# Optimization experiments

Hardware: AMD Instinct MI355X
Metric: run time of the kernel (lower is better)

Reference implementation:

```python
import jax, jax.numpy as jnp
import numpy as np

D_MODEL = 1024
HEADS = 16


def setup_inputs() -> dict:
    key = jax.random.key(0)
    ks = jax.random.split(key, 11)
    B, S, D = 2, 2048, D_MODEL
    scale = 1.0 / np.sqrt(D)
    inp = {
        "q": jax.random.normal(ks[0], (B, S, D), jnp.float32),
        "k": jax.random.normal(ks[1], (B, S, D), jnp.float32),
        "v": jax.random.normal(ks[2], (B, S, D), jnp.float32),
        "w_q": jax.random.normal(ks[3], (D, D), jnp.float32) * scale,
        "b_q": jnp.zeros((D,), jnp.float32),
        "w_k": jax.random.normal(ks[4], (D, D), jnp.float32) * scale,
        "b_k": jnp.zeros((D,), jnp.float32),
        "w_v": jax.random.normal(ks[5], (D, D), jnp.float32) * scale,
        "b_v": jnp.zeros((D,), jnp.float32),
        "w_o": jax.random.normal(ks[6], (D, D), jnp.float32) * scale,
        "b_o": jnp.zeros((D,), jnp.float32),
    }
    return inp


def reference(q, k, v, w_q, b_q, w_k, b_k, w_v, b_v, w_o, b_o):
    B, S, D = q.shape
    H = HEADS
    Dh = D // H

    def split(x):  # [B,S,D] -> [B,H,S,Dh]
        return x.reshape(B, S, H, Dh).transpose(0, 2, 1, 3)

    qh = split(q @ w_q + b_q)
    kh = split(k @ w_k + b_k)
    vh = split(v @ w_v + b_v)

    # scaled dot-product attention: softmax(Q K^T / sqrt(Dh)) V
    scores = jnp.einsum("bhsd,bhtd->bhst", qh, kh) / jnp.sqrt(
        jnp.asarray(Dh, qh.dtype)
    )
    attn = jax.nn.softmax(scores, axis=-1)
    out = jnp.einsum("bhst,bhtd->bhsd", attn, vh)

    concat = out.transpose(0, 2, 1, 3).reshape(B, S, D)
    return concat @ w_o + b_o
```

## Files before the change

kernel.cpp:

```cpp
#include <hip/hip_runtime.h>
#include <hip/hip_bf16.h>
#include <math.h>

using bf16 = __hip_bfloat16;
typedef __bf16 bf16x8v __attribute__((ext_vector_type(8)));
typedef float f32x4v __attribute__((ext_vector_type(4)));

#define AS1 __attribute__((address_space(1)))
#define AS3 __attribute__((address_space(3)))

__device__ __forceinline__ void g2l16(const void* g, void* l) {
  __builtin_amdgcn_global_load_lds((const AS1 void*)g, (AS3 void*)l, 16, 0, 0);
}

__device__ __forceinline__ float fclamp(float v) {
  return fminf(fmaxf(v, -6.0e4f), 6.0e4f);
}

__device__ __forceinline__ unsigned packbf(float a, float b) {
  unsigned short lo = __builtin_bit_cast(unsigned short, __float2bfloat16(a));
  unsigned short hi = __builtin_bit_cast(unsigned short, __float2bfloat16(b));
  return (unsigned)lo | ((unsigned)hi << 16);
}

#define QSCL 0.1803368801111204f

__global__ __launch_bounds__(256) void transpose_cvt4(
    const float* __restrict__ w0, const float* __restrict__ w1,
    const float* __restrict__ w2, const float* __restrict__ w3,
    bf16* __restrict__ o0, bf16* __restrict__ o1,
    bf16* __restrict__ o2, bf16* __restrict__ o3) {
  const float* in = (blockIdx.z == 0) ? w0 : (blockIdx.z == 1) ? w1
                    : (blockIdx.z == 2) ? w2 : w3;
  bf16* out = (blockIdx.z == 0) ? o0 : (blockIdx.z == 1) ? o1
              : (blockIdx.z == 2) ? o2 : o3;
  __shared__ alignas(16) bf16 tile[64][80];
  const int t = threadIdx.x;
  const int bx = blockIdx.x * 64, by = blockIdx.y * 64;
#pragma unroll
  for (int p = 0; p < 4; ++p) {
    int idx = p * 1024 + t * 4;
    int r = idx >> 6, c0 = idx & 63;
    float4 v = *(const float4*)&in[(size_t)(by + r) * 1024 + bx + c0];
    tile[c0 + 0][r] = __float2bfloat16(v.x);
    tile[c0 + 1][r] = __float2bfloat16(v.y);
    tile[c0 + 2][r] = __float2bfloat16(v.z);
    tile[c0 + 3][r] = __float2bfloat16(v.w);
  }
  __syncthreads();
#pragma unroll
  for (int p = 0; p < 2; ++p) {
    int idx = p * 2048 + t * 8;
    int c = idx >> 6, r0 = idx & 63;
    *(uint4*)&out[(size_t)(bx + c) * 1024 + by + r0] = *(const uint4*)&tile[c][r0];
  }
}

__global__ __launch_bounds__(256, 2) void gemm_qkv(
    const float* __restrict__ Aq, const float* __restrict__ Ak,
    const float* __restrict__ Av,
    const bf16* __restrict__ WtQ, const bf16* __restrict__ WtK,
    const bf16* __restrict__ WtV,
    const float* __restrict__ bq, const float* __restrict__ bk_,
    const float* __restrict__ bv_,
    bf16* __restrict__ Qh, bf16* __restrict__ Kh, bf16* __restrict__ Vt) {
  constexpr int K = 1024, LDA = 40;
  const int z = blockIdx.z;
  const float* A  = (z == 0) ? Aq : (z == 1) ? Ak : Av;
  const bf16* Bt  = (z == 0) ? WtQ : (z == 1) ? WtK : WtV;
  const float* bias = (z == 0) ? bq : (z == 1) ? bk_ : bv_;
  bf16* C = (z == 0) ? Qh : (z == 1) ? Kh : Vt;

  __shared__ alignas(16) bf16 As[2][128 * LDA];
  __shared__ alignas(16) bf16 Bs[2][128 * 32];
  const int t = threadIdx.x;
  const int wave = t >> 6, lane = t & 63;
  const int quad = lane >> 4, l16 = lane & 15;
  const int bm = blockIdx.x * 128, bn = blockIdx.y * 128;
  const int wm = (wave & 1) * 64, wn = (wave >> 1) * 64;

  f32x4v acc[4][4] = {};

  auto loadA = [&](int k0, float4* f) {
#pragma unroll
    for (int c = 0; c < 2; ++c) {
      int idx = c * 2048 + t * 8;
      int row = idx >> 5, col = idx & 31;
      const float* src = &A[(size_t)(bm + row) * K + k0 + col];
      f[c * 2 + 0] = *(const float4*)src;
      f[c * 2 + 1] = *(const float4*)(src + 4);
    }
  };
  auto writeA = [&](int buf, const float4* f) {
#pragma unroll
    for (int c = 0; c < 2; ++c) {
      int idx = c * 2048 + t * 8;
      int row = idx >> 5, col = idx & 31;
      uint4 u;
      u.x = packbf(f[c * 2 + 0].x, f[c * 2 + 0].y);
      u.y = packbf(f[c * 2 + 0].z, f[c * 2 + 0].w);
      u.z = packbf(f[c * 2 + 1].x, f[c * 2 + 1].y);
      u.w = packbf(f[c * 2 + 1].z, f[c * 2 + 1].w);
      *(uint4*)&As[buf][row * LDA + col] = u;
    }
  };
  auto stageB = [&](int k0, int buf) {
#pragma unroll
    for (int c = 0; c < 2; ++c) {
      int idx = c * 2048 + t * 8;
      int row = idx >> 5, col = idx & 31;
      g2l16(&Bt[(size_t)(bn + row) * K + k0 + col],
            &Bs[buf][c * 2048 + wave * 512]);
    }
  };

  {
    float4 f0[4];
    loadA(0, f0);
    stageB(0, 0);
    writeA(0, f0);
    __syncthreads();
  }

  int buf = 0;
  for (int k0 = 0; k0 < K; k0 += 32) {
    const bool more = (k0 + 32) < K;
    float4 fN[4];
    if (more) {
      loadA(k0 + 32, fN);
      stageB(k0 + 32, buf ^ 1);
    }

    bf16x8v a[4], b[4];
#pragma unroll
    for (int mi = 0; mi < 4; ++mi)
      a[mi] = *(const bf16x8v*)&As[buf][(wm + mi * 16 + l16) * LDA + quad * 8];
#pragma unroll
    for (int ni = 0; ni < 4; ++ni)
      b[ni] = *(const bf16x8v*)&Bs[buf][(wn + ni * 16 + l16) * 32 + quad * 8];
#pragma unroll
    for (int mi = 0; mi < 4; ++mi)
#pragma unroll
      for (int ni = 0; ni < 4; ++ni)
        acc[mi][ni] = __builtin_amdgcn_mfma_f32_16x16x32_bf16(a[mi], b[ni],
                                                              acc[mi][ni], 0, 0, 0);

    if (more) writeA(buf ^ 1, fN);
    __syncthreads();
    buf ^= 1;
  }

  if (z == 2) {
#pragma unroll
    for (int ni = 0; ni < 4; ++ni) {
      int n = bn + wn + ni * 16 + l16;
      float bz = bias[n];
      int h_ = n >> 6, d_ = n & 63;
#pragma unroll
      for (int mi = 0; mi < 4; ++mi) {
        int m0 = bm + wm + mi * 16 + quad * 4;
        int b_ = m0 >> 11, s0 = m0 & 2047;
        uint2 u;
        u.x = packbf(fclamp(acc[mi][ni][0] + bz), fclamp(acc[mi][ni][1] + bz));
        u.y = packbf(fclamp(acc[mi][ni][2] + bz), fclamp(acc[mi][ni][3] + bz));
        *(uint2*)&C[((size_t)(b_ * 16 + h_) * 64 + d_) * 2048 + s0] = u;
      }
    }
  } else {
    const float scl = (z == 0) ? QSCL : 1.0f;
#pragma unroll
    for (int ni = 0; ni < 4; ++ni) {
      int n = bn + wn + ni * 16 + l16;
      float bz = bias[n];
      int h_ = n >> 6, d_ = n & 63;
#pragma unroll
      for (int mi = 0; mi < 4; ++mi)
#pragma unroll
        for (int r = 0; r < 4; ++r) {
          int m = bm + wm + mi * 16 + quad * 4 + r;
          int b_ = m >> 11, s_ = m & 2047;
          C[((size_t)(b_ * 16 + h_) * 2048 + s_) * 64 + d_] =
              __float2bfloat16(fclamp(acc[mi][ni][r] + bz) * scl);
        }
    }
  }
}

__global__ __launch_bounds__(256, 2) void gemm_out(
    const bf16* __restrict__ A, const bf16* __restrict__ Bt,
    const float* __restrict__ bias, float* __restrict__ C) {
  constexpr int K = 1024, N = 1024;
  __shared__ alignas(16) bf16 As[2][128 * 32];
  __shared__ alignas(16) bf16 Bs[2][64 * 32];
  const int t = threadIdx.x;
  const int wave = t >> 6, lane = t & 63;
  const int quad = lane >> 4, l16 = lane & 15;
  const int bm = blockIdx.x * 128, bn = blockIdx.y * 64;
  const int wm = (wave & 1) * 64, wn = (wave >> 1) * 32;

  f32x4v acc[4][2] = {};

  auto stage = [&](int k0, int buf) {
#pragma unroll
    for (int c = 0; c < 2; ++c) {
      int idx = c * 2048 + t * 8;
      int row = idx >> 5, col = idx & 31;
      g2l16(&A[(size_t)(bm + row) * K + k0 + col],
            &As[buf][c * 2048 + wave * 512]);
    }
    {
      int idx = t * 8;
      int row = idx >> 5, col = idx & 31;
      g2l16(&Bt[(size_t)(bn + row) * K + k0 + col], &Bs[buf][wave * 512]);
    }
  };

  stage(0, 0);
  __syncthreads();

  int buf = 0;
  for (int k0 = 0; k0 < K; k0 += 32) {
    if (k0 + 32 < K) stage(k0 + 32, buf ^ 1);

    bf16x8v a[4], b[2];
#pragma unroll
    for (int mi = 0; mi < 4; ++mi)
      a[mi] = *(const bf16x8v*)&As[buf][(wm + mi * 16 + l16) * 32 + quad * 8];
#pragma unroll
    for (int ni = 0; ni < 2; ++ni)
      b[ni] = *(const bf16x8v*)&Bs[buf][(wn + ni * 16 + l16) * 32 + quad * 8];
#pragma unroll
    for (int mi = 0; mi < 4; ++mi)
#pragma unroll
      for (int ni = 0; ni < 2; ++ni)
        acc[mi][ni] = __builtin_amdgcn_mfma_f32_16x16x32_bf16(a[mi], b[ni],
                                                              acc[mi][ni], 0, 0, 0);
    __syncthreads();
    buf ^= 1;
  }

#pragma unroll
  for (int ni = 0; ni < 2; ++ni) {
    int n = bn + wn + ni * 16 + l16;
    float bz = bias[n];
#pragma unroll
    for (int mi = 0; mi < 4; ++mi)
#pragma unroll
      for (int r = 0; r < 4; ++r) {
        int m = bm + wm + mi * 16 + quad * 4 + r;
        C[(size_t)m * N + n] = fclamp(acc[mi][ni][r] + bz);
      }
  }
}

__global__ __launch_bounds__(512, 4) void attn(
    const bf16* __restrict__ Qh, const bf16* __restrict__ Kh,
    const bf16* __restrict__ Vt, bf16* __restrict__ Ctx) {
  constexpr int LDPP = 40;
  __shared__ alignas(16) bf16 QsPs[128 * 64];
  __shared__ alignas(16) bf16 Ks[3][64 * 64];
  __shared__ alignas(16) bf16 Vs[3][64 * 64];
  const int t = threadIdx.x;
  const int wave = t >> 6, lane = t & 63;
  const int quad = lane >> 4, l16 = lane & 15;
  const int sw = l16 & 7;

  const int lin = blockIdx.x;
  const int li = lin >> 3;
  const int qb = li & 15;
  const int bh = (lin & 7) * 4 + (li >> 4);

  const size_t bh_off = (size_t)bh * 2048 * 64;
  const bf16* Qb = Qh + bh_off;
  const bf16* Kb = Kh + bh_off;
  const bf16* Vb = Vt + bh_off;

  const int srow = t >> 3;
  const int schunk = t & 7;

  auto stageKV = [&](int kt, int buf) {
    int mc = schunk ^ (srow & 7);
    g2l16(&Kb[(size_t)(kt * 64 + srow) * 64 + mc * 8], &Ks[buf][wave * 512]);
    g2l16(&Vb[(size_t)srow * 2048 + kt * 64 + mc * 8], &Vs[buf][wave * 512]);
  };

#pragma unroll
  for (int c = 0; c < 2; ++c) {
    int row = c * 64 + srow;
    int mc = schunk ^ (row & 7);
    g2l16(&Qb[(size_t)(qb * 128 + row) * 64 + mc * 8],
          &QsPs[c * 4096 + wave * 512]);
  }
  stageKV(0, 0);
  asm volatile("s_waitcnt vmcnt(2)" ::: "memory");
  __builtin_amdgcn_s_barrier();

  bf16x8v aq[2];
#pragma unroll
  for (int kk = 0; kk < 2; ++kk)
    aq[kk] = *(const bf16x8v*)
        &QsPs[(wave * 16 + l16) * 64 + (((kk * 4 + quad) ^ sw) << 3)];

  __syncthreads();
  bf16* Psw = QsPs + wave * (16 * LDPP);

  stageKV(1, 1);

  bf16x8v vone;
#pragma unroll
  for (int i = 0; i < 8; ++i) vone[i] = (__bf16)1.0f;

  f32x4v lsum = {};
  f32x4v oacc[4] = {};

  auto compute = [&](int buf) {
#pragma unroll
    for (int h = 0; h < 2; ++h) {
      f32x4v s[2] = {};
      __builtin_amdgcn_s_setprio(1);
#pragma unroll
      for (int kk = 0; kk < 2; ++kk)
#pragma unroll
        for (int ni = 0; ni < 2; ++ni) {
          bf16x8v bk = *(const bf16x8v*)
              &Ks[buf][(h * 32 + ni * 16 + l16) * 64 + (((kk * 4 + quad) ^ sw) << 3)];
          s[ni] = __builtin_amdgcn_mfma_f32_16x16x32_bf16(bk, aq[kk],
                                                          s[ni], 0, 0, 0);
        }
      __builtin_amdgcn_s_setprio(0);

#pragma unroll
      for (int ni = 0; ni < 2; ++ni) {
        float p0 = __builtin_amdgcn_exp2f(fminf(s[ni][0], 80.f));
        float p1 = __builtin_amdgcn_exp2f(fminf(s[ni][1], 80.f));
        float p2 = __builtin_amdgcn_exp2f(fminf(s[ni][2], 80.f));
        float p3 = __builtin_amdgcn_exp2f(fminf(s[ni][3], 80.f));
        uint2 u;
        u.x = packbf(p0, p1);
        u.y = packbf(p2, p3);
        *(uint2*)&Psw[l16 * LDPP + ni * 16 + quad * 4] = u;
      }

      bf16x8v ap = *(const bf16x8v*)&Psw[l16 * LDPP + quad * 8];
      __builtin_amdgcn_s_setprio(1);
      lsum = __builtin_amdgcn_mfma_f32_16x16x32_bf16(ap, vone, lsum, 0, 0, 0);
#pragma unroll
      for (int ni = 0; ni < 4; ++ni) {
        bf16x8v bv = *(const bf16x8v*)
            &Vs[buf][(ni * 16 + l16) * 64 + (((h * 4 + quad) ^ sw) << 3)];
        oacc[ni] = __builtin_amdgcn_mfma_f32_16x16x32_bf16(ap, bv, oacc[ni],
                                                           0, 0, 0);
      }
      __builtin_amdgcn_s_setprio(0);
    }
  };

  int bufc = 0;
  for (int tt = 0; tt < 30; ++tt) {
    int bufs = bufc + 2; if (bufs >= 3) bufs -= 3;
    stageKV(tt + 2, bufs);
    compute(bufc);
    asm volatile("s_waitcnt vmcnt(2)" ::: "memory");
    __builtin_amdgcn_s_barrier();
    bufc = (bufc == 2) ? 0 : bufc + 1;
  }
  compute(bufc);
  asm volatile("s_waitcnt vmcnt(0)" ::: "memory");
  __builtin_amdgcn_s_barrier();
  bufc = (bufc == 2) ? 0 : bufc + 1;
  compute(bufc);

  const int b_ = bh >> 4, h_ = bh & 15;
#pragma unroll
  for (int r = 0; r < 4; ++r) {
    int sr = qb * 128 + wave * 16 + quad * 4 + r;
    float inv = 1.0f / fmaxf(lsum[r], 1.0e-20f);
#pragma unroll
    for (int ni = 0; ni < 4; ++ni) {
      int col = h_ * 64 + ni * 16 + l16;
      Ctx[(size_t)(b_ * 2048 + sr) * 1024 + col] =
          __float2bfloat16(fclamp(oacc[ni][r] * inv));
    }
  }
}

extern "C" void kernel_launch(void* const* d_in, const int* in_sizes, int n_in,
                              void* d_out, int out_size, void* d_ws, size_t ws_size,
                              hipStream_t stream) {
  const float* q   = (const float*)d_in[0];
  const float* k   = (const float*)d_in[1];
  const float* v   = (const float*)d_in[2];
  const float* w_q = (const float*)d_in[3];
  const float* b_q = (const float*)d_in[4];
  const float* w_k = (const float*)d_in[5];
  const float* b_k = (const float*)d_in[6];
  const float* w_v = (const float*)d_in[7];
  const float* b_v = (const float*)d_in[8];
  const float* w_o = (const float*)d_in[9];
  const float* b_o = (const float*)d_in[10];
  float* out = (float*)d_out;

  char* ws = (char*)d_ws;
  const size_t MB = (size_t)1024 * 1024;
  bf16* WtQ = (bf16*)(ws + 0 * MB);
  bf16* WtK = (bf16*)(ws + 2 * MB);
  bf16* WtV = (bf16*)(ws + 4 * MB);
  bf16* WtO = (bf16*)(ws + 6 * MB);
  bf16* Qh  = (bf16*)(ws + 8 * MB);
  bf16* Kh  = (bf16*)(ws + 16 * MB);
  bf16* Vt  = (bf16*)(ws + 24 * MB);
  bf16* Ctx = (bf16*)(ws + 32 * MB);

  dim3 tb(256);
  transpose_cvt4<<<dim3(16, 16, 4), tb, 0, stream>>>(w_q, w_k, w_v, w_o,
                                                     WtQ, WtK, WtV, WtO);
  gemm_qkv<<<dim3(32, 8, 3), tb, 0, stream>>>(q, k, v, WtQ, WtK, WtV,
                                              b_q, b_k, b_v, Qh, Kh, Vt);
  attn<<<dim3(512), dim3(512), 0, stream>>>(Qh, Kh, Vt, Ctx);
  gemm_out<<<dim3(32, 16), tb, 0, stream>>>(Ctx, WtO, b_o, out);
}
```

Measured before the change: 241.3 us.

## Pre-convert QKV inputs to bf16 and triple-buffer GEMM LDS pipelines

Adds a separate kernel that converts the fp32 q/k/v activations to bf16, so the QKV GEMM can stage A tiles with direct global-to-LDS loads instead of register loads and in-loop packing. Both GEMMs move from double to triple buffering, using explicit vmcnt waits and raw barriers so two stages stay in flight. The cost is an extra kernel launch plus a full write and re-read of the converted inputs, more LDS per block, and an unpadded A layout that may bring back LDS bank conflicts.

```diff
diff --git a/kernel.cpp b/kernel.cpp
--- a/kernel.cpp
+++ b/kernel.cpp
@@ -56,23 +56,38 @@
   }
 }
 
-__global__ __launch_bounds__(256, 2) void gemm_qkv(
-    const float* __restrict__ Aq, const float* __restrict__ Ak,
-    const float* __restrict__ Av,
+__global__ __launch_bounds__(256) void cvt3(
+    const float* __restrict__ q, const float* __restrict__ k,
+    const float* __restrict__ v, bf16* __restrict__ oq,
+    bf16* __restrict__ ok, bf16* __restrict__ ov) {
+  const float* in = (blockIdx.y == 0) ? q : (blockIdx.y == 1) ? k : v;
+  bf16* out = (blockIdx.y == 0) ? oq : (blockIdx.y == 1) ? ok : ov;
+  int i = (blockIdx.x * 256 + threadIdx.x) * 8;
+  float4 a = *(const float4*)&in[i];
+  float4 b = *(const float4*)&in[i + 4];
+  uint4 u;
+  u.x = packbf(a.x, a.y); u.y = packbf(a.z, a.w);
+  u.z = packbf(b.x, b.y); u.w = packbf(b.z, b.w);
+  *(uint4*)&out[i] = u;
+}
+
+__global__ __launch_bounds__(256, 2) void gemm_qkv_bf16(
+    const bf16* __restrict__ Aq, const bf16* __restrict__ Ak,
+    const bf16* __restrict__ Av,
     const bf16* __restrict__ WtQ, const bf16* __restrict__ WtK,
     const bf16* __restrict__ WtV,
     const float* __restrict__ bq, const float* __restrict__ bk_,
     const float* __restrict__ bv_,
     bf16* __restrict__ Qh, bf16* __restrict__ Kh, bf16* __restrict__ Vt) {
-  constexpr int K = 1024, LDA = 40;
+  constexpr int K = 1024;
   const int z = blockIdx.z;
-  const float* A  = (z == 0) ? Aq : (z == 1) ? Ak : Av;
-  const bf16* Bt  = (z == 0) ? WtQ : (z == 1) ? WtK : WtV;
+  const bf16* A    = (z == 0) ? Aq : (z == 1) ? Ak : Av;
+  const bf16* Bt   = (z == 0) ? WtQ : (z == 1) ? WtK : WtV;
   const float* bias = (z == 0) ? bq : (z == 1) ? bk_ : bv_;
   bf16* C = (z == 0) ? Qh : (z == 1) ? Kh : Vt;
 
-  __shared__ alignas(16) bf16 As[2][128 * LDA];
-  __shared__ alignas(16) bf16 Bs[2][128 * 32];
+  __shared__ alignas(16) bf16 As[3][128 * 32];
+  __shared__ alignas(16) bf16 Bs[3][128 * 32];
   const int t = threadIdx.x;
   const int wave = t >> 6, lane = t & 63;
   const int quad = lane >> 4, l16 = lane & 15;
@@ -81,60 +96,22 @@
 
   f32x4v acc[4][4] = {};
 
-  auto loadA = [&](int k0, float4* f) {
+  auto stage = [&](int ks, int buf) {
+    int k0 = ks * 32;
 #pragma unroll
     for (int c = 0; c < 2; ++c) {
       int idx = c * 2048 + t * 8;
       int row = idx >> 5, col = idx & 31;
-      const float* src = &A[(size_t)(bm + row) * K + k0 + col];
-      f[c * 2 + 0] = *(const float4*)src;
-      f[c * 2 + 1] = *(const float4*)(src + 4);
-    }
-  };
-  auto writeA = [&](int buf, const float4* f) {
-#pragma unroll
-    for (int c = 0; c < 2; ++c) {
-      int idx = c * 2048 + t * 8;
-      int row = idx >> 5, col = idx & 31;
-      uint4 u;
-      u.x = packbf(f[c * 2 + 0].x, f[c * 2 + 0].y);
-      u.y = packbf(f[c * 2 + 0].z, f[c * 2 + 0].w);
-      u.z = packbf(f[c * 2 + 1].x, f[c * 2 + 1].y);
-      u.w = packbf(f[c * 2 + 1].z, f[c * 2 + 1].w);
-      *(uint4*)&As[buf][row * LDA + col] = u;
-    }
-  };
-  auto stageB = [&](int k0, int buf) {
-#pragma unroll
-    for (int c = 0; c < 2; ++c) {
-      int idx = c * 2048 + t * 8;
-      int row = idx >> 5, col = idx & 31;
-      g2l16(&Bt[(size_t)(bn + row) * K + k0 + col],
-            &Bs[buf][c * 2048 + wave * 512]);
-    }
-  };
-
-  {
-    float4 f0[4];
-    loadA(0, f0);
-    stageB(0, 0);
-    writeA(0, f0);
-    __syncthreads();
-  }
-
-  int buf = 0;
-  for (int k0 = 0; k0 < K; k0 += 32) {
-    const bool more = (k0 + 32) < K;
-    float4 fN[4];
-    if (more) {
-      loadA(k0 + 32, fN);
-      stageB(k0 + 32, buf ^ 1);
-    }
-
+      g2l16(&A[(size_t)(bm + row) * K + k0 + col], &As[buf][c * 2048 + wave * 512]);
+      g2l16(&Bt[(size_t)(bn + row) * K + k0 + col], &Bs[buf][c * 2048 + wave * 512]);
+    }
+  };
+
+  auto compute = [&](int buf) {
     bf16x8v a[4], b[4];
 #pragma unroll
     for (int mi = 0; mi < 4; ++mi)
-      a[mi] = *(const bf16x8v*)&As[buf][(wm + mi * 16 + l16) * LDA + quad * 8];
+      a[mi] = *(const bf16x8v*)&As[buf][(wm + mi * 16 + l16) * 32 + quad * 8];
 #pragma unroll
     for (int ni = 0; ni < 4; ++ni)
       b[ni] = *(const bf16x8v*)&Bs[buf][(wn + ni * 16 + l16) * 32 + quad * 8];
@@ -144,11 +121,27 @@
       for (int ni = 0; ni < 4; ++ni)
         acc[mi][ni] = __builtin_amdgcn_mfma_f32_16x16x32_bf16(a[mi], b[ni],
                                                               acc[mi][ni], 0, 0, 0);
-
-    if (more) writeA(buf ^ 1, fN);
-    __syncthreads();
-    buf ^= 1;
-  }
+  };
+
+  stage(0, 0);
+  asm volatile("s_waitcnt vmcnt(0)" ::: "memory");
+  __builtin_amdgcn_s_barrier();
+  stage(1, 1);
+
+  int bufc = 0;
+  for (int tt = 0; tt < 30; ++tt) {
+    int bufs = bufc + 2; if (bufs >= 3) bufs -= 3;
+    stage(tt + 2, bufs);
+    compute(bufc);
+    asm volatile("s_waitcnt vmcnt(4)" ::: "memory");
+    __builtin_amdgcn_s_barrier();
+    bufc = (bufc == 2) ? 0 : bufc + 1;
+  }
+  compute(bufc);
+  asm volatile("s_waitcnt vmcnt(0)" ::: "memory");
+  __builtin_amdgcn_s_barrier();
+  bufc = (bufc == 2) ? 0 : bufc + 1;
+  compute(bufc);
 
   if (z == 2) {
 #pragma unroll
@@ -190,8 +183,8 @@
     const bf16* __restrict__ A, const bf16* __restrict__ Bt,
     const float* __restrict__ bias, float* __restrict__ C) {
   constexpr int K = 1024, N = 1024;
-  __shared__ alignas(16) bf16 As[2][128 * 32];
-  __shared__ alignas(16) bf16 Bs[2][64 * 32];
+  __shared__ alignas(16) bf16 As[3][128 * 32];
+  __shared__ alignas(16) bf16 Bs[3][64 * 32];
   const int t = threadIdx.x;
   const int wave = t >> 6, lane = t & 63;
   const int quad = lane >> 4, l16 = lane & 15;
@@ -200,13 +193,13 @@
 
   f32x4v acc[4][2] = {};
 
-  auto stage = [&](int k0, int buf) {
+  auto stage = [&](int ks, int buf) {
+    int k0 = ks * 32;
 #pragma unroll
     for (int c = 0; c < 2; ++c) {
       int idx = c * 2048 + t * 8;
       int row = idx >> 5, col = idx & 31;
-      g2l16(&A[(size_t)(bm + row) * K + k0 + col],
-            &As[buf][c * 2048 + wave * 512]);
+      g2l16(&A[(size_t)(bm + row) * K + k0 + col], &As[buf][c * 2048 + wave * 512]);
     }
     {
       int idx = t * 8;
@@ -215,13 +208,7 @@
     }
   };
 
-  stage(0, 0);
-  __syncthreads();
-
-  int buf = 0;
-  for (int k0 = 0; k0 < K; k0 += 32) {
-    if (k0 + 32 < K) stage(k0 + 32, buf ^ 1);
-
+  auto compute = [&](int buf) {
     bf16x8v a[4], b[2];
 #pragma unroll
     for (int mi = 0; mi < 4; ++mi)
@@ -235,9 +222,27 @@
       for (int ni = 0; ni < 2; ++ni)
         acc[mi][ni] = __builtin_amdgcn_mfma_f32_16x16x32_bf16(a[mi], b[ni],
                                                               acc[mi][ni], 0, 0, 0);
-    __syncthreads();
-    buf ^= 1;
-  }
+  };
+
+  stage(0, 0);
+  asm volatile("s_waitcnt vmcnt(0)" ::: "memory");
+  __builtin_amdgcn_s_barrier();
+  stage(1, 1);
+
+  int bufc = 0;
+  for (int tt = 0; tt < 30; ++tt) {
+    int bufs = bufc + 2; if (bufs >= 3) bufs -= 3;
+    stage(tt + 2, bufs);
+    compute(bufc);
+    asm volatile("s_waitcnt vmcnt(3)" ::: "memory");
+    __builtin_amdgcn_s_barrier();
+    bufc = (bufc == 2) ? 0 : bufc + 1;
+  }
+  compute(bufc);
+  asm volatile("s_waitcnt vmcnt(0)" ::: "memory");
+  __builtin_amdgcn_s_barrier();
+  bufc = (bufc == 2) ? 0 : bufc + 1;
+  compute(bufc);
 
 #pragma unroll
   for (int ni = 0; ni < 2; ++ni) {
@@ -406,16 +411,20 @@
   bf16* WtK = (bf16*)(ws + 2 * MB);
   bf16* WtV = (bf16*)(ws + 4 * MB);
   bf16* WtO = (bf16*)(ws + 6 * MB);
-  bf16* Qh  = (bf16*)(ws + 8 * MB);
-  bf16* Kh  = (bf16*)(ws + 16 * MB);
-  bf16* Vt  = (bf16*)(ws + 24 * MB);
-  bf16* Ctx = (bf16*)(ws + 32 * MB);
+  bf16* Qa  = (bf16*)(ws + 8 * MB);
+  bf16* Ka  = (bf16*)(ws + 16 * MB);
+  bf16* Va  = (bf16*)(ws + 24 * MB);
+  bf16* Qh  = (bf16*)(ws + 32 * MB);
+  bf16* Kh  = (bf16*)(ws + 40 * MB);
+  bf16* Vt  = (bf16*)(ws + 48 * MB);
+  bf16* Ctx = Qa;
 
   dim3 tb(256);
   transpose_cvt4<<<dim3(16, 16, 4), tb, 0, stream>>>(w_q, w_k, w_v, w_o,
                                                      WtQ, WtK, WtV, WtO);
-  gemm_qkv<<<dim3(32, 8, 3), tb, 0, stream>>>(q, k, v, WtQ, WtK, WtV,
-                                              b_q, b_k, b_v, Qh, Kh, Vt);
+  cvt3<<<dim3(2048, 3), tb, 0, stream>>>(q, k, v, Qa, Ka, Va);
+  gemm_qkv_bf16<<<dim3(32, 8, 3), tb, 0, stream>>>(Qa, Ka, Va, WtQ, WtK, WtV,
+                                                   b_q, b_k, b_v, Qh, Kh, Vt);
   attn<<<dim3(512), dim3(512), 0, stream>>>(Qh, Kh, Vt, Ctx);
   gemm_out<<<dim3(32, 16), tb, 0, stream>>>(Ctx, WtO, b_o, out);
 }
```

Measured after the change: 224.6 us. 1.07x faster.
